# Kernel tuning notes

Measured on AMD Instinct MI355X. Metric: run time of the kernel, lower is better.

The kernel has to match this reference:

```python
import jax, jax.numpy as jnp
import numpy as np

L, B, H, R = 128, 4, 768, 97
LN_EPS = 1e-5


def setup_inputs() -> dict:
    key = jax.random.key(0)
    ks = jax.random.split(key, 8)
    s = 0.02
    return {
        "h_re1": jax.random.normal(ks[0], (L, B, H), jnp.float32),
        "h_re2": jax.random.normal(ks[1], (L, B, H), jnp.float32),
        "mask": jax.random.uniform(ks[2], (L, B), jnp.float32),
        "Wr": jax.random.normal(ks[3], (H, 2 * H), jnp.float32) * s,
        "br": jnp.zeros((H,), jnp.float32),
        "Wh": jax.random.normal(ks[4], (H, 3 * H), jnp.float32) * s,
        "bh": jnp.zeros((H,), jnp.float32),
        "gamma": jnp.ones((H,), jnp.float32),
        "beta": jnp.zeros((H,), jnp.float32),
        "Wo": jax.random.normal(ks[5], (R, H), jnp.float32) * s,
        "bo": jnp.zeros((R,), jnp.float32),
    }


def reference(h_re1, h_re2, mask, Wr, br, Wh, bh, gamma, beta, Wo, bo):
    # h_re1, h_re2: [L, B, H]; mask: [L, B]
    h = h_re2.shape[-1]
    # global context: tanh(Linear(cat(h_re1,h_re2))), max over length -> [B, H]
    g = jnp.tanh(jnp.einsum('lbi,hi->lbh', jnp.concatenate([h_re1, h_re2], axis=-1), Wr) + br)
    g = jnp.max(g, axis=0)  # [B, H]
    # hid2hid(cat(r1, r2, g)) == r1 @ W1.T + r2 @ W2.T + g @ W3.T + b
    # (avoids materializing the [L,L,B,3H] repeat+cat tensor)
    W1, W2, W3 = Wh[:, :h], Wh[:, h:2 * h], Wh[:, 2 * h:]
    a = jnp.einsum('lbi,hi->lbh', h_re2, W1)          # varies over first pair axis
    b2 = jnp.einsum('lbi,hi->lbh', h_re2, W2)         # varies over second pair axis
    gp = jnp.einsum('bi,hi->bh', g, W3) + bh          # constant over pairs
    pre = a[:, None, :, :] + b2[None, :, :, :] + gp   # [L, L, B, H]
    # LayerNorm over last dim (biased variance, as in torch)
    mu = jnp.mean(pre, axis=-1, keepdims=True)
    var = jnp.var(pre, axis=-1, keepdims=True)
    x = (pre - mu) * jax.lax.rsqrt(var + LN_EPS) * gamma + beta
    x = jax.nn.elu(x)  # dropout is identity in eval mode
    out = jax.nn.sigmoid(jnp.einsum('klbh,rh->klbr', x, Wo) + bo)  # [L, L, B, R]
    # pairwise mask: mask_e1 * mask_e2, broadcast over relation dim
    m = mask[:, None, :, None] * mask[None, :, :, None]
    return out * m
```

## Files before the change

### kernel.cpp

```cpp
#include <hip/hip_runtime.h>
#include <hip/hip_bf16.h>
#include <stdint.h>

#define L_ 128
#define B_ 4
#define H_ 768
#define R_ 97
#define LN_EPS 1e-5f

typedef _Float16 f16x8 __attribute__((ext_vector_type(8)));
typedef _Float16 f16x4 __attribute__((ext_vector_type(4)));
typedef _Float16 f16x2 __attribute__((ext_vector_type(2)));
typedef float f32x4 __attribute__((ext_vector_type(4)));

extern "C" __device__ _Float16 __ocml_exp2_f16(_Float16);

__device__ inline f16x8 cvt8(float4 v0, float4 v1) {
  f16x8 o;
  o[0] = (_Float16)v0.x; o[1] = (_Float16)v0.y; o[2] = (_Float16)v0.z; o[3] = (_Float16)v0.w;
  o[4] = (_Float16)v1.x; o[5] = (_Float16)v1.y; o[6] = (_Float16)v1.z; o[7] = (_Float16)v1.w;
  return o;
}

__global__ __launch_bounds__(256) void prep_all(const float* __restrict__ h1,
                                                const float* __restrict__ h2,
                                                const float* __restrict__ Wr,
                                                const float* __restrict__ Wh,
                                                const float* __restrict__ Wo,
                                                const float* __restrict__ gamma,
                                                const float* __restrict__ beta,
                                                _Float16* __restrict__ ccH,
                                                _Float16* __restrict__ BpR,
                                                _Float16* __restrict__ BpW,
                                                _Float16* __restrict__ WoP,
                                                _Float16* __restrict__ gbH,
                                                unsigned int* __restrict__ gmaxU) {
  int blk = blockIdx.x;
  if (blk < 512) {
    const float2* s1 = (const float2*)(h1 + (size_t)blk * H_);
    const float2* s2 = (const float2*)(h2 + (size_t)blk * H_);
    f16x2* d = (f16x2*)(ccH + (size_t)blk * (2 * H_));
    for (int i = threadIdx.x; i < H_ / 2; i += 256) {
      float2 v = s1[i]; f16x2 o; o[0] = (_Float16)v.x; o[1] = (_Float16)v.y; d[i] = o;
    }
    for (int i = threadIdx.x; i < H_ / 2; i += 256) {
      float2 v = s2[i]; f16x2 o; o[0] = (_Float16)v.x; o[1] = (_Float16)v.y; d[H_ / 2 + i] = o;
    }
    return;
  }
  blk -= 512;
  if (blk < 576) {
    int c = blk * 256 + threadIdx.x;
    int l = c & 63, u = c >> 6;
    int nt = u % 48, ks = u / 48;
    int n = nt * 16 + (l & 15);
    int k = ks * 32 + ((l >> 4) << 3);
    const float4* s = (const float4*)(Wr + (size_t)n * 1536 + k);
    *(f16x8*)(BpR + (size_t)c * 8) = cvt8(s[0], s[1]);
    return;
  }
  blk -= 576;
  if (blk < 576) {
    int c = blk * 256 + threadIdx.x;
    int l = c & 63, u = c >> 6;
    int nt = u % 96, ks = u / 96;
    int n = nt * 16 + (l & 15);
    int k = ks * 32 + ((l >> 4) << 3);
    const float* src = (n < 768) ? (Wh + (size_t)n * 2304 + k)
                                 : (Wh + (size_t)(n - 768) * 2304 + 768 + k);
    const float4* s = (const float4*)src;
    *(f16x8*)(BpW + (size_t)c * 8) = cvt8(s[0], s[1]);
    return;
  }
  blk -= 576;
  if (blk < 48) {
    int c = blk * 256 + threadIdx.x;
    int l = c & 63, u = c >> 6;
    int nt = u & 7, ks = u >> 3;
    int n = nt * 16 + (l & 15);
    int k = ks * 32 + ((l >> 4) << 3);
    f16x8 o = {};
    if (n < R_) {
      const float4* s = (const float4*)(Wo + (size_t)n * 768 + k);
      o = cvt8(s[0], s[1]);
    }
    *(f16x8*)(WoP + (size_t)c * 8) = o;
    return;
  }
  blk -= 48;
  if (blk < 3) {
    int i = blk * 256 + threadIdx.x;
    if (i < H_) {
      gbH[i] = (_Float16)gamma[i];
      gbH[H_ + i] = (_Float16)beta[i];
    }
    return;
  }
  blk -= 3;
  int i = blk * 256 + threadIdx.x;
  if (i < B_ * H_) gmaxU[i] = 0u;
}

__device__ __forceinline__ void gemm_g_tile(int nb, int mb,
                                            const _Float16* __restrict__ A,
                                            const _Float16* __restrict__ BpR,
                                            const float* __restrict__ br,
                                            unsigned int* __restrict__ gmaxU) {
  int w = threadIdx.x >> 6, l = threadIdx.x & 63;
  int row0 = mb * 32 + (w & 1) * 16;
  int nt0 = nb * 4 + (w >> 1) * 2;
  const f16x8* ap = (const f16x8*)(A + (size_t)(row0 + (l & 15)) * 1536 + (l >> 4) * 8);
  const f16x8* bp = (const f16x8*)(BpR + ((size_t)nt0 * 64 + l) * 8);
  f32x4 acc0 = {}, acc1 = {};
  f16x8 ac = ap[0], b0c = bp[0], b1c = bp[64];
  for (int ks = 0; ks < 48; ++ks) {
    f16x8 an = {}, b0n = {}, b1n = {};
    if (ks < 47) {
      an = ap[(ks + 1) * 4];
      b0n = bp[(size_t)(ks + 1) * 3072];
      b1n = bp[(size_t)(ks + 1) * 3072 + 64];
    }
    acc0 = __builtin_amdgcn_mfma_f32_16x16x32_f16(ac, b0c, acc0, 0, 0, 0);
    acc1 = __builtin_amdgcn_mfma_f32_16x16x32_f16(ac, b1c, acc1, 0, 0, 0);
    ac = an; b0c = b0n; b1c = b1n;
  }
#pragma unroll
  for (int q = 0; q < 2; ++q) {
    f32x4 acc = q ? acc1 : acc0;
    int col = nb * 64 + (w >> 1) * 32 + q * 16 + (l & 15);
#pragma unroll
    for (int r = 0; r < 4; ++r) {
      int row = row0 + (l >> 4) * 4 + r;
      float t = tanhf(acc[r] + br[col]) + 1.0f;
      atomicMax(&gmaxU[(row & 3) * H_ + col], __float_as_uint(t));
    }
  }
}

__device__ __forceinline__ void gemm_ab_tile(int nb, int mb,
                                             const _Float16* __restrict__ ccH,
                                             const _Float16* __restrict__ BpW,
                                             _Float16* __restrict__ aH,
                                             _Float16* __restrict__ bH) {
  int w = threadIdx.x >> 6, l = threadIdx.x & 63;
  int row0 = mb * 32 + (w & 1) * 16;
  int nt0 = nb * 4 + (w >> 1) * 2;
  const f16x8* ap = (const f16x8*)(ccH + (size_t)(row0 + (l & 15)) * 1536 + 768 + (l >> 4) * 8);
  const f16x8* bp = (const f16x8*)(BpW + ((size_t)nt0 * 64 + l) * 8);
  f32x4 acc0 = {}, acc1 = {};
  f16x8 ac = ap[0], b0c = bp[0], b1c = bp[64];
  for (int ks = 0; ks < 24; ++ks) {
    f16x8 an = {}, b0n = {}, b1n = {};
    if (ks < 23) {
      an = ap[(ks + 1) * 4];
      b0n = bp[(size_t)(ks + 1) * 6144];
      b1n = bp[(size_t)(ks + 1) * 6144 + 64];
    }
    acc0 = __builtin_amdgcn_mfma_f32_16x16x32_f16(ac, b0c, acc0, 0, 0, 0);
    acc1 = __builtin_amdgcn_mfma_f32_16x16x32_f16(ac, b1c, acc1, 0, 0, 0);
    ac = an; b0c = b0n; b1c = b1n;
  }
#pragma unroll
  for (int q = 0; q < 2; ++q) {
    f32x4 acc = q ? acc1 : acc0;
    int col = nb * 64 + (w >> 1) * 32 + q * 16 + (l & 15);
#pragma unroll
    for (int r = 0; r < 4; ++r) {
      int row = row0 + (l >> 4) * 4 + r;
      float v = acc[r];
      if (col < 768) aH[(size_t)row * H_ + col] = (_Float16)v;
      else           bH[(size_t)row * H_ + (col - 768)] = (_Float16)v;
    }
  }
}

__global__ __launch_bounds__(256) void gemm_both(const _Float16* __restrict__ ccH,
                                                 const _Float16* __restrict__ BpR,
                                                 const _Float16* __restrict__ BpW,
                                                 const float* __restrict__ br,
                                                 unsigned int* __restrict__ gmaxU,
                                                 _Float16* __restrict__ aH,
                                                 _Float16* __restrict__ bH) {
  int bid = blockIdx.x;
  if (bid < 192) {
    gemm_g_tile(bid % 12, bid / 12, ccH, BpR, br, gmaxU);
  } else {
    int j2 = bid - 192;
    gemm_ab_tile(j2 % 24, j2 / 24, ccH, BpW, aH, bH);
  }
}

__global__ __launch_bounds__(256) void gp_kernel(const float* __restrict__ Wh,
                                                 const unsigned int* __restrict__ gmaxU,
                                                 const float* __restrict__ bh,
                                                 float* __restrict__ gpv) {
  int n = blockIdx.x;
  int w = threadIdx.x >> 6, l = threadIdx.x & 63;
  const float* wr = Wh + (size_t)n * 2304 + 1536;
  const unsigned int* gm = gmaxU + (size_t)w * H_;
  float s = 0.f;
#pragma unroll
  for (int t = 0; t < 12; ++t) {
    int i = l + 64 * t;
    s += wr[i] * (__uint_as_float(gm[i]) - 1.0f);
  }
#pragma unroll
  for (int off = 32; off; off >>= 1) s += __shfl_xor(s, off);
  if (l == 0) gpv[(size_t)w * H_ + n] = s + bh[n];
}

__global__ __launch_bounds__(256) void stats(const _Float16* __restrict__ aH,
                                             const _Float16* __restrict__ bH,
                                             const float* __restrict__ gpv,
                                             _Float16* __restrict__ aH2,
                                             float* __restrict__ S,
                                             float* __restrict__ Q) {
  int r = blockIdx.x * 4 + (threadIdx.x >> 6);
  int l = threadIdx.x & 63;
  float s = 0.f, q = 0.f;
  if (r < 512) {
    int b = r & 3;
    const f16x4* ap = (const f16x4*)(aH + (size_t)r * H_);
    const float4* gp4 = (const float4*)(gpv + (size_t)b * H_);
    f16x4* op = (f16x4*)(aH2 + (size_t)r * H_);
#pragma unroll
    for (int t = 0; t < 3; ++t) {
      int i = t * 64 + l;
      f16x4 av = ap[i];
      float4 g4 = gp4[i];
      f16x4 o;
      o[0] = (_Float16)((float)av[0] + g4.x);
      o[1] = (_Float16)((float)av[1] + g4.y);
      o[2] = (_Float16)((float)av[2] + g4.z);
      o[3] = (_Float16)((float)av[3] + g4.w);
      op[i] = o;
#pragma unroll
      for (int j = 0; j < 4; ++j) { float y = (float)o[j]; s += y; q += y * y; }
    }
  } else {
    const f16x4* bp = (const f16x4*)(bH + (size_t)(r - 512) * H_);
#pragma unroll
    for (int t = 0; t < 3; ++t) {
      f16x4 bv = bp[t * 64 + l];
#pragma unroll
      for (int j = 0; j < 4; ++j) { float y = (float)bv[j]; s += y; q += y * y; }
    }
  }
#pragma unroll
  for (int off = 32; off; off >>= 1) {
    s += __shfl_xor(s, off);
    q += __shfl_xor(q, off);
  }
  if (l == 0) { S[r] = s; Q[r] = q; }
}

__global__ __launch_bounds__(256) void dotab(const _Float16* __restrict__ aH2,
                                             const _Float16* __restrict__ bH,
                                             const float* __restrict__ S,
                                             const float* __restrict__ Q,
                                             float* __restrict__ mu_arr,
                                             float* __restrict__ rs_arr) {
  int w = threadIdx.x >> 6, l = threadIdx.x & 63;
  int ltq = blockIdx.x, kt = blockIdx.y, b = blockIdx.z;
  int lt = ltq * 4 + w;
  const f16x8* ap = (const f16x8*)(aH2 + ((size_t)(kt * 16 + (l & 15)) * 4 + b) * H_ + (l >> 4) * 8);
  const f16x8* bp = (const f16x8*)(bH + ((size_t)(lt * 16 + (l & 15)) * 4 + b) * H_ + (l >> 4) * 8);
  f32x4 acc = {};
  f16x8 a0 = ap[0], b0 = bp[0], a1 = ap[4], b1 = bp[4];
  for (int ks = 0; ks < 24; ++ks) {
    f16x8 a2 = {}, b2 = {};
    if (ks < 22) { a2 = ap[(ks + 2) * 4]; b2 = bp[(ks + 2) * 4]; }
    acc = __builtin_amdgcn_mfma_f32_16x16x32_f16(a0, b0, acc, 0, 0, 0);
    a0 = a1; b0 = b1; a1 = a2; b1 = b2;
  }
#pragma unroll
  for (int r = 0; r < 4; ++r) {
    int k = kt * 16 + (l >> 4) * 4 + r;
    int lg = lt * 16 + (l & 15);
    int arow = k * 4 + b, brow = lg * 4 + b;
    float mu = (S[arow] + S[512 + brow]) * (1.f / H_);
    float q2 = Q[arow] + Q[512 + brow] + 2.f * acc[r];
    float var = fmaxf(q2 * (1.f / H_) - mu * mu, 0.f);
    float rs = rsqrtf(var + LN_EPS);
    size_t idx = (size_t)k * 512 + (size_t)lg * 4 + b;
    mu_arr[idx] = mu;
    rs_arr[idx] = rs;
  }
}

__global__ __launch_bounds__(256) void fused2(const _Float16* __restrict__ aH2,
                                              const _Float16* __restrict__ bH,
                                              const _Float16* __restrict__ gbH,
                                              const _Float16* __restrict__ WoP,
                                              const float* __restrict__ bo,
                                              const float* __restrict__ mask,
                                              const float* __restrict__ mu_arr,
                                              const float* __restrict__ rs_arr,
                                              float* __restrict__ out) {
  __shared__ __align__(16) uint4 WoLds[2048];
  int tid = threadIdx.x, w = tid >> 6, l = tid & 63;
  int m0 = blockIdx.x * 64;
  int myrow = m0 + w * 16 + (l & 15);
  int b = myrow & 3, li = (myrow >> 2) & 127, kk = myrow >> 9;
  const f16x8* ap = (const f16x8*)(aH2 + ((size_t)kk * 4 + b) * H_ + (l >> 4) * 8);
  const f16x8* bp = (const f16x8*)(bH + ((size_t)li * 4 + b) * H_ + (l >> 4) * 8);
  const f16x8* gp8 = (const f16x8*)(gbH + (l >> 4) * 8);
  const f16x8* be8 = (const f16x8*)(gbH + H_ + (l >> 4) * 8);
  float mu = mu_arr[myrow], rs = rs_arr[myrow];
  _Float16 muh = (_Float16)mu, rsh = (_Float16)rs;
  _Float16 l2e = (_Float16)1.44269504f;
  f16x8 mu8, rs8, zero8, one8, l2e8;
#pragma unroll
  for (int j = 0; j < 8; ++j) {
    mu8[j] = muh; rs8[j] = rsh;
    zero8[j] = (_Float16)0.f; one8[j] = (_Float16)1.f; l2e8[j] = l2e;
  }

  const uint4* wog = (const uint4*)WoP;
  f16x8 a8 = ap[0], b8 = bp[0], g8 = gp8[0], e8 = be8[0];

  f32x4 acc[7] = {};
  for (int ph = 0; ph < 6; ++ph) {
    __syncthreads();
    const uint4* gsrc = wog + (size_t)ph * 2048;
#pragma unroll
    for (int g = 0; g < 2; ++g) {
      uint4 v0 = gsrc[(g * 4 + 0) * 256 + tid];
      uint4 v1 = gsrc[(g * 4 + 1) * 256 + tid];
      uint4 v2 = gsrc[(g * 4 + 2) * 256 + tid];
      uint4 v3 = gsrc[(g * 4 + 3) * 256 + tid];
      WoLds[(g * 4 + 0) * 256 + tid] = v0;
      WoLds[(g * 4 + 1) * 256 + tid] = v1;
      WoLds[(g * 4 + 2) * 256 + tid] = v2;
      WoLds[(g * 4 + 3) * 256 + tid] = v3;
    }
    __syncthreads();
#pragma unroll
    for (int s = 0; s < 4; ++s) {
      int ks = ph * 4 + s;
      f16x8 an = {}, bn = {}, gn = {}, en = {};
      if (ks < 23) {
        an = ap[(ks + 1) * 4];
        bn = bp[(ks + 1) * 4];
        gn = gp8[(ks + 1) * 4];
        en = be8[(ks + 1) * 4];
      }
      f16x8 x = a8 + b8;
      f16x8 c1 = rs8 * g8;
      f16x8 yv = (x - mu8) * c1 + e8;
      f16x8 y2 = yv * l2e8;
      f16x8 ex;
#pragma unroll
      for (int j = 0; j < 8; ++j) ex[j] = __ocml_exp2_f16(y2[j]);
      ex = ex - one8;
      f16x8 av = __builtin_elementwise_max(yv, zero8) + __builtin_elementwise_min(ex, zero8);
      const f16x8* bvp = (const f16x8*)&WoLds[s * 512];
#pragma unroll
      for (int q = 0; q < 7; ++q) {
        f16x8 bv = bvp[q * 64 + l];
        acc[q] = __builtin_amdgcn_mfma_f32_16x16x32_f16(av, bv, acc[q], 0, 0, 0);
      }
      a8 = an; b8 = bn; g8 = gn; e8 = en;
    }
  }
  float mv[4];
#pragma unroll
  for (int r = 0; r < 4; ++r) {
    int row = m0 + w * 16 + (l >> 4) * 4 + r;
    int bb = row & 3, ll = (row >> 2) & 127, kx = row >> 9;
    mv[r] = mask[kx * 4 + bb] * mask[ll * 4 + bb];
  }
#pragma unroll
  for (int q = 0; q < 7; ++q) {
    int col = q * 16 + (l & 15);
    if (col < R_) {
      float bov = bo[col];
#pragma unroll
      for (int r = 0; r < 4; ++r) {
        int row = m0 + w * 16 + (l >> 4) * 4 + r;
        float z = acc[q][r] + bov;
        out[(size_t)row * R_ + col] = mv[r] / (1.f + __expf(-z));
      }
    }
  }
}

extern "C" void kernel_launch(void* const* d_in, const int* in_sizes, int n_in,
                              void* d_out, int out_size, void* d_ws, size_t ws_size,
                              hipStream_t stream) {
  const float* h1    = (const float*)d_in[0];
  const float* h2    = (const float*)d_in[1];
  const float* mask  = (const float*)d_in[2];
  const float* Wr    = (const float*)d_in[3];
  const float* br    = (const float*)d_in[4];
  const float* Wh    = (const float*)d_in[5];
  const float* bh    = (const float*)d_in[6];
  const float* gamma = (const float*)d_in[7];
  const float* beta  = (const float*)d_in[8];
  const float* Wo    = (const float*)d_in[9];
  const float* bo    = (const float*)d_in[10];
  float* out = (float*)d_out;
  char* ws = (char*)d_ws;

  _Float16* ccH = (_Float16*)ws;                    size_t off = 512 * 1536 * 2;
  _Float16* BpR = (_Float16*)(ws + off);            off += (size_t)1536 * 768 * 2;
  _Float16* BpW = (_Float16*)(ws + off);            off += (size_t)768 * 1536 * 2;
  _Float16* WoP = (_Float16*)(ws + off);            off += 768 * 128 * 2;
  _Float16* gbH = (_Float16*)(ws + off);            off += 4096;
  _Float16* aH  = (_Float16*)(ws + off);            off += 512 * 768 * 2;
  _Float16* bH  = (_Float16*)(ws + off);            off += 512 * 768 * 2;
  _Float16* aH2 = (_Float16*)(ws + off);            off += 512 * 768 * 2;
  unsigned int* gmaxU = (unsigned int*)(ws + off);  off += 3072 * 4;
  float* gpv = (float*)(ws + off);                  off += 3072 * 4;
  float* S   = (float*)(ws + off);                  off += 1024 * 4;
  float* Q   = (float*)(ws + off);                  off += 1024 * 4;
  float* mu_arr = (float*)(ws + off);               off += 65536 * 4;
  float* rs_arr = (float*)(ws + off);               off += 65536 * 4;

  prep_all<<<512 + 576 + 576 + 48 + 3 + 12, 256, 0, stream>>>(h1, h2, Wr, Wh, Wo, gamma, beta,
                                                              ccH, BpR, BpW, WoP, gbH, gmaxU);

  gemm_both<<<576, 256, 0, stream>>>(ccH, BpR, BpW, br, gmaxU, aH, bH);
  gp_kernel<<<768, 256, 0, stream>>>(Wh, gmaxU, bh, gpv);
  stats<<<256, 256, 0, stream>>>(aH, bH, gpv, aH2, S, Q);
  dotab<<<dim3(2, 8, 4), 256, 0, stream>>>(aH2, bH, S, Q, mu_arr, rs_arr);

  fused2<<<1024, 256, 0, stream>>>(aH2, bH, gbH, WoP, bo, mask, mu_arr, rs_arr, out);
}
```

Before: 92.12 us.

## Fuse LayerNorm statistics into the output kernel, dropping stats and dotab launches

Removes the separate stats and dotab kernels. Each fused3 block now computes the per-row sums, squared sums and a-b dot products for its 64 pair rows directly from aH, bH and an fp16 gp vector, then derives mean and rstd in-block. The gp vector is added inside the main loop rather than pre-materialised into aH2. This saves two launches and the mu/rs round trip through global memory. In exchange every block redundantly recomputes stats with a serial 48-iteration loop per thread, and gp is now rounded to fp16 before the add.

```diff
diff --git a/kernel.cpp b/kernel.cpp
--- a/kernel.cpp
+++ b/kernel.cpp
@@ -193,7 +193,7 @@
 __global__ __launch_bounds__(256) void gp_kernel(const float* __restrict__ Wh,
                                                  const unsigned int* __restrict__ gmaxU,
                                                  const float* __restrict__ bh,
-                                                 float* __restrict__ gpv) {
+                                                 _Float16* __restrict__ gpH) {
   int n = blockIdx.x;
   int w = threadIdx.x >> 6, l = threadIdx.x & 63;
   const float* wr = Wh + (size_t)n * 2304 + 1536;
@@ -206,107 +206,83 @@
   }
 #pragma unroll
   for (int off = 32; off; off >>= 1) s += __shfl_xor(s, off);
-  if (l == 0) gpv[(size_t)w * H_ + n] = s + bh[n];
-}
-
-__global__ __launch_bounds__(256) void stats(const _Float16* __restrict__ aH,
-                                             const _Float16* __restrict__ bH,
-                                             const float* __restrict__ gpv,
-                                             _Float16* __restrict__ aH2,
-                                             float* __restrict__ S,
-                                             float* __restrict__ Q) {
-  int r = blockIdx.x * 4 + (threadIdx.x >> 6);
-  int l = threadIdx.x & 63;
-  float s = 0.f, q = 0.f;
-  if (r < 512) {
-    int b = r & 3;
-    const f16x4* ap = (const f16x4*)(aH + (size_t)r * H_);
-    const float4* gp4 = (const float4*)(gpv + (size_t)b * H_);
-    f16x4* op = (f16x4*)(aH2 + (size_t)r * H_);
-#pragma unroll
-    for (int t = 0; t < 3; ++t) {
-      int i = t * 64 + l;
-      f16x4 av = ap[i];
-      float4 g4 = gp4[i];
-      f16x4 o;
-      o[0] = (_Float16)((float)av[0] + g4.x);
-      o[1] = (_Float16)((float)av[1] + g4.y);
-      o[2] = (_Float16)((float)av[2] + g4.z);
-      o[3] = (_Float16)((float)av[3] + g4.w);
-      op[i] = o;
-#pragma unroll
-      for (int j = 0; j < 4; ++j) { float y = (float)o[j]; s += y; q += y * y; }
-    }
-  } else {
-    const f16x4* bp = (const f16x4*)(bH + (size_t)(r - 512) * H_);
-#pragma unroll
-    for (int t = 0; t < 3; ++t) {
-      f16x4 bv = bp[t * 64 + l];
-#pragma unroll
-      for (int j = 0; j < 4; ++j) { float y = (float)bv[j]; s += y; q += y * y; }
-    }
-  }
-#pragma unroll
-  for (int off = 32; off; off >>= 1) {
-    s += __shfl_xor(s, off);
-    q += __shfl_xor(q, off);
-  }
-  if (l == 0) { S[r] = s; Q[r] = q; }
-}
-
-__global__ __launch_bounds__(256) void dotab(const _Float16* __restrict__ aH2,
-                                             const _Float16* __restrict__ bH,
-                                             const float* __restrict__ S,
-                                             const float* __restrict__ Q,
-                                             float* __restrict__ mu_arr,
-                                             float* __restrict__ rs_arr) {
-  int w = threadIdx.x >> 6, l = threadIdx.x & 63;
-  int ltq = blockIdx.x, kt = blockIdx.y, b = blockIdx.z;
-  int lt = ltq * 4 + w;
-  const f16x8* ap = (const f16x8*)(aH2 + ((size_t)(kt * 16 + (l & 15)) * 4 + b) * H_ + (l >> 4) * 8);
-  const f16x8* bp = (const f16x8*)(bH + ((size_t)(lt * 16 + (l & 15)) * 4 + b) * H_ + (l >> 4) * 8);
-  f32x4 acc = {};
-  f16x8 a0 = ap[0], b0 = bp[0], a1 = ap[4], b1 = bp[4];
-  for (int ks = 0; ks < 24; ++ks) {
-    f16x8 a2 = {}, b2 = {};
-    if (ks < 22) { a2 = ap[(ks + 2) * 4]; b2 = bp[(ks + 2) * 4]; }
-    acc = __builtin_amdgcn_mfma_f32_16x16x32_f16(a0, b0, acc, 0, 0, 0);
-    a0 = a1; b0 = b1; a1 = a2; b1 = b2;
-  }
-#pragma unroll
-  for (int r = 0; r < 4; ++r) {
-    int k = kt * 16 + (l >> 4) * 4 + r;
-    int lg = lt * 16 + (l & 15);
-    int arow = k * 4 + b, brow = lg * 4 + b;
-    float mu = (S[arow] + S[512 + brow]) * (1.f / H_);
-    float q2 = Q[arow] + Q[512 + brow] + 2.f * acc[r];
-    float var = fmaxf(q2 * (1.f / H_) - mu * mu, 0.f);
-    float rs = rsqrtf(var + LN_EPS);
-    size_t idx = (size_t)k * 512 + (size_t)lg * 4 + b;
-    mu_arr[idx] = mu;
-    rs_arr[idx] = rs;
-  }
-}
-
-__global__ __launch_bounds__(256) void fused2(const _Float16* __restrict__ aH2,
+  if (l == 0) gpH[(size_t)w * H_ + n] = (_Float16)(s + bh[n]);
+}
+
+__global__ __launch_bounds__(256) void fused3(const _Float16* __restrict__ aH,
                                               const _Float16* __restrict__ bH,
+                                              const _Float16* __restrict__ gpH,
                                               const _Float16* __restrict__ gbH,
                                               const _Float16* __restrict__ WoP,
                                               const float* __restrict__ bo,
                                               const float* __restrict__ mask,
-                                              const float* __restrict__ mu_arr,
-                                              const float* __restrict__ rs_arr,
                                               float* __restrict__ out) {
   __shared__ __align__(16) uint4 WoLds[2048];
+  __shared__ float SA[4], QA[4], pS[64], pQ[64], pD[64];
   int tid = threadIdx.x, w = tid >> 6, l = tid & 63;
   int m0 = blockIdx.x * 64;
-  int myrow = m0 + w * 16 + (l & 15);
-  int b = myrow & 3, li = (myrow >> 2) & 127, kk = myrow >> 9;
-  const f16x8* ap = (const f16x8*)(aH2 + ((size_t)kk * 4 + b) * H_ + (l >> 4) * 8);
+  int kk = m0 >> 9;
+  int li0 = (m0 >> 2) & 127;
+
+  {
+    const f16x4* ar = (const f16x4*)(aH + ((size_t)(kk * 4 + w)) * H_);
+    const f16x4* gr = (const f16x4*)(gpH + (size_t)w * H_);
+    float s = 0.f, q = 0.f;
+#pragma unroll
+    for (int t = 0; t < 3; ++t) {
+      int i = t * 64 + l;
+      f16x4 a4 = ar[i], g4 = gr[i];
+#pragma unroll
+      for (int j = 0; j < 4; ++j) {
+        float x = (float)a4[j] + (float)g4[j];
+        s += x; q += x * x;
+      }
+    }
+#pragma unroll
+    for (int off = 32; off; off >>= 1) { s += __shfl_xor(s, off); q += __shfl_xor(q, off); }
+    if (l == 0) { SA[w] = s; QA[w] = q; }
+  }
+  {
+    int p = tid >> 2, sub = tid & 3;
+    int lig = p & 15;
+    int pb = (p >> 4);
+    int li = li0 + (p >> 2);
+    int b = p & 3;
+    (void)lig; (void)pb;
+    const f16x4* brp = (const f16x4*)(bH + ((size_t)li * 4 + b) * H_);
+    const f16x4* arp = (const f16x4*)(aH + ((size_t)(kk * 4 + b)) * H_);
+    const f16x4* grp = (const f16x4*)(gpH + (size_t)b * H_);
+    float sb = 0.f, qb = 0.f, d = 0.f;
+    for (int i = 0; i < 48; ++i) {
+      int idx = sub + 4 * i;
+      f16x4 b4 = brp[idx], a4 = arp[idx], g4 = grp[idx];
+#pragma unroll
+      for (int j = 0; j < 4; ++j) {
+        float bv = (float)b4[j];
+        float av = (float)a4[j] + (float)g4[j];
+        sb += bv; qb += bv * bv; d += av * bv;
+      }
+    }
+    sb += __shfl_xor(sb, 1); sb += __shfl_xor(sb, 2);
+    qb += __shfl_xor(qb, 1); qb += __shfl_xor(qb, 2);
+    d  += __shfl_xor(d, 1);  d  += __shfl_xor(d, 2);
+    if (sub == 0) { pS[p] = sb; pQ[p] = qb; pD[p] = d; }
+  }
+  __syncthreads();
+  int rr = w * 16 + (l & 15);
+  int b = rr & 3;
+  int pair = rr;
+  float mu = (SA[b] + pS[pair]) * (1.f / H_);
+  float q2 = QA[b] + pQ[pair] + 2.f * pD[pair];
+  float var = fmaxf(q2 * (1.f / H_) - mu * mu, 0.f);
+  float rs = rsqrtf(var + LN_EPS);
+
+  int li = li0 + (rr >> 2);
+  const f16x8* ap = (const f16x8*)(aH + ((size_t)(kk * 4 + b)) * H_ + (l >> 4) * 8);
   const f16x8* bp = (const f16x8*)(bH + ((size_t)li * 4 + b) * H_ + (l >> 4) * 8);
+  const f16x8* gpp = (const f16x8*)(gpH + (size_t)b * H_ + (l >> 4) * 8);
   const f16x8* gp8 = (const f16x8*)(gbH + (l >> 4) * 8);
   const f16x8* be8 = (const f16x8*)(gbH + H_ + (l >> 4) * 8);
-  float mu = mu_arr[myrow], rs = rs_arr[myrow];
   _Float16 muh = (_Float16)mu, rsh = (_Float16)rs;
   _Float16 l2e = (_Float16)1.44269504f;
   f16x8 mu8, rs8, zero8, one8, l2e8;
@@ -317,7 +293,7 @@
   }
 
   const uint4* wog = (const uint4*)WoP;
-  f16x8 a8 = ap[0], b8 = bp[0], g8 = gp8[0], e8 = be8[0];
+  f16x8 a8 = ap[0], b8 = bp[0], p8 = gpp[0], g8 = gp8[0], e8 = be8[0];
 
   f32x4 acc[7] = {};
   for (int ph = 0; ph < 6; ++ph) {
@@ -338,14 +314,15 @@
 #pragma unroll
     for (int s = 0; s < 4; ++s) {
       int ks = ph * 4 + s;
-      f16x8 an = {}, bn = {}, gn = {}, en = {};
+      f16x8 an = {}, bn = {}, pn = {}, gn = {}, en = {};
       if (ks < 23) {
         an = ap[(ks + 1) * 4];
         bn = bp[(ks + 1) * 4];
+        pn = gpp[(ks + 1) * 4];
         gn = gp8[(ks + 1) * 4];
         en = be8[(ks + 1) * 4];
       }
-      f16x8 x = a8 + b8;
+      f16x8 x = (a8 + b8) + p8;
       f16x8 c1 = rs8 * g8;
       f16x8 yv = (x - mu8) * c1 + e8;
       f16x8 y2 = yv * l2e8;
@@ -360,7 +337,7 @@
         f16x8 bv = bvp[q * 64 + l];
         acc[q] = __builtin_amdgcn_mfma_f32_16x16x32_f16(av, bv, acc[q], 0, 0, 0);
       }
-      a8 = an; b8 = bn; g8 = gn; e8 = en;
+      a8 = an; b8 = bn; p8 = pn; g8 = gn; e8 = en;
     }
   }
   float mv[4];
@@ -409,21 +386,14 @@
   _Float16* gbH = (_Float16*)(ws + off);            off += 4096;
   _Float16* aH  = (_Float16*)(ws + off);            off += 512 * 768 * 2;
   _Float16* bH  = (_Float16*)(ws + off);            off += 512 * 768 * 2;
-  _Float16* aH2 = (_Float16*)(ws + off);            off += 512 * 768 * 2;
   unsigned int* gmaxU = (unsigned int*)(ws + off);  off += 3072 * 4;
-  float* gpv = (float*)(ws + off);                  off += 3072 * 4;
-  float* S   = (float*)(ws + off);                  off += 1024 * 4;
-  float* Q   = (float*)(ws + off);                  off += 1024 * 4;
-  float* mu_arr = (float*)(ws + off);               off += 65536 * 4;
-  float* rs_arr = (float*)(ws + off);               off += 65536 * 4;
+  _Float16* gpH = (_Float16*)(ws + off);            off += 4 * 768 * 2;
 
   prep_all<<<512 + 576 + 576 + 48 + 3 + 12, 256, 0, stream>>>(h1, h2, Wr, Wh, Wo, gamma, beta,
                                                               ccH, BpR, BpW, WoP, gbH, gmaxU);
 
   gemm_both<<<576, 256, 0, stream>>>(ccH, BpR, BpW, br, gmaxU, aH, bH);
-  gp_kernel<<<768, 256, 0, stream>>>(Wh, gmaxU, bh, gpv);
-  stats<<<256, 256, 0, stream>>>(aH, bH, gpv, aH2, S, Q);
-  dotab<<<dim3(2, 8, 4), 256, 0, stream>>>(aH2, bH, S, Q, mu_arr, rs_arr);
-
-  fused2<<<1024, 256, 0, stream>>>(aH2, bH, gbH, WoP, bo, mask, mu_arr, rs_arr, out);
-}
+  gp_kernel<<<768, 256, 0, stream>>>(Wh, gmaxU, bh, gpH);
+
+  fused3<<<1024, 256, 0, stream>>>(aH, bH, gpH, gbH, WoP, bo, mask, out);
+}
```

New measurement: 124.7 us. 35.4% more time.

## Process two 16-row tiles per wave in fused2 to reuse staged Wo

Applied to the files above, without the earlier changes.

Each block of fused2 now covers 128 rows instead of 64, with every wave computing two 16-row MFMA tiles that share each Wo fragment read from LDS. The grid halves to 512 blocks, so the global-to-LDS staging of Wo is done half as often per row. The software prefetch of the next k-slice of a/b/gamma/beta is dropped in favour of direct loads in the loop. The cost is doubled accumulator registers, which may lower occupancy and expose load latency.

```diff
diff --git a/kernel.cpp b/kernel.cpp
--- a/kernel.cpp
+++ b/kernel.cpp
@@ -299,27 +299,33 @@
                                               float* __restrict__ out) {
   __shared__ __align__(16) uint4 WoLds[2048];
   int tid = threadIdx.x, w = tid >> 6, l = tid & 63;
-  int m0 = blockIdx.x * 64;
-  int myrow = m0 + w * 16 + (l & 15);
-  int b = myrow & 3, li = (myrow >> 2) & 127, kk = myrow >> 9;
-  const f16x8* ap = (const f16x8*)(aH2 + ((size_t)kk * 4 + b) * H_ + (l >> 4) * 8);
-  const f16x8* bp = (const f16x8*)(bH + ((size_t)li * 4 + b) * H_ + (l >> 4) * 8);
+  int m0 = blockIdx.x * 128;
+  int kk = m0 >> 9;
+  int row0 = m0 + w * 32 + (l & 15);
+  int row1 = row0 + 16;
+  int b0 = row0 & 3, li0 = (row0 >> 2) & 127;
+  int b1 = row1 & 3, li1 = (row1 >> 2) & 127;
+  const f16x8* ap0 = (const f16x8*)(aH2 + ((size_t)kk * 4 + b0) * H_ + (l >> 4) * 8);
+  const f16x8* bp0 = (const f16x8*)(bH + ((size_t)li0 * 4 + b0) * H_ + (l >> 4) * 8);
+  const f16x8* ap1 = (const f16x8*)(aH2 + ((size_t)kk * 4 + b1) * H_ + (l >> 4) * 8);
+  const f16x8* bp1 = (const f16x8*)(bH + ((size_t)li1 * 4 + b1) * H_ + (l >> 4) * 8);
   const f16x8* gp8 = (const f16x8*)(gbH + (l >> 4) * 8);
   const f16x8* be8 = (const f16x8*)(gbH + H_ + (l >> 4) * 8);
-  float mu = mu_arr[myrow], rs = rs_arr[myrow];
-  _Float16 muh = (_Float16)mu, rsh = (_Float16)rs;
+  float mu0f = mu_arr[row0], rs0f = rs_arr[row0];
+  float mu1f = mu_arr[row1], rs1f = rs_arr[row1];
   _Float16 l2e = (_Float16)1.44269504f;
-  f16x8 mu8, rs8, zero8, one8, l2e8;
+  f16x8 mu80, rs80, mu81, rs81, zero8, one8, l2e8;
 #pragma unroll
   for (int j = 0; j < 8; ++j) {
-    mu8[j] = muh; rs8[j] = rsh;
+    mu80[j] = (_Float16)mu0f; rs80[j] = (_Float16)rs0f;
+    mu81[j] = (_Float16)mu1f; rs81[j] = (_Float16)rs1f;
     zero8[j] = (_Float16)0.f; one8[j] = (_Float16)1.f; l2e8[j] = l2e;
   }
 
   const uint4* wog = (const uint4*)WoP;
-  f16x8 a8 = ap[0], b8 = bp[0], g8 = gp8[0], e8 = be8[0];
-
-  f32x4 acc[7] = {};
+
+  f32x4 acc0[7] = {};
+  f32x4 acc1[7] = {};
   for (int ph = 0; ph < 6; ++ph) {
     __syncthreads();
     const uint4* gsrc = wog + (size_t)ph * 2048;
@@ -338,48 +344,60 @@
 #pragma unroll
     for (int s = 0; s < 4; ++s) {
       int ks = ph * 4 + s;
-      f16x8 an = {}, bn = {}, gn = {}, en = {};
-      if (ks < 23) {
-        an = ap[(ks + 1) * 4];
-        bn = bp[(ks + 1) * 4];
-        gn = gp8[(ks + 1) * 4];
-        en = be8[(ks + 1) * 4];
+      f16x8 a80 = ap0[ks * 4];
+      f16x8 b80 = bp0[ks * 4];
+      f16x8 a81 = ap1[ks * 4];
+      f16x8 b81 = bp1[ks * 4];
+      f16x8 g8 = gp8[ks * 4];
+      f16x8 e8 = be8[ks * 4];
+      f16x8 x0 = a80 + b80;
+      f16x8 x1 = a81 + b81;
+      f16x8 c10 = rs80 * g8;
+      f16x8 c11 = rs81 * g8;
+      f16x8 yv0 = (x0 - mu80) * c10 + e8;
+      f16x8 yv1 = (x1 - mu81) * c11 + e8;
+      f16x8 y20 = yv0 * l2e8;
+      f16x8 y21 = yv1 * l2e8;
+      f16x8 ex0, ex1;
+#pragma unroll
+      for (int j = 0; j < 8; ++j) {
+        ex0[j] = __ocml_exp2_f16(y20[j]);
+        ex1[j] = __ocml_exp2_f16(y21[j]);
       }
-      f16x8 x = a8 + b8;
-      f16x8 c1 = rs8 * g8;
-      f16x8 yv = (x - mu8) * c1 + e8;
-      f16x8 y2 = yv * l2e8;
-      f16x8 ex;
-#pragma unroll
-      for (int j = 0; j < 8; ++j) ex[j] = __ocml_exp2_f16(y2[j]);
-      ex = ex - one8;
-      f16x8 av = __builtin_elementwise_max(yv, zero8) + __builtin_elementwise_min(ex, zero8);
+      ex0 = ex0 - one8;
+      ex1 = ex1 - one8;
+      f16x8 av0 = __builtin_elementwise_max(yv0, zero8) + __builtin_elementwise_min(ex0, zero8);
+      f16x8 av1 = __builtin_elementwise_max(yv1, zero8) + __builtin_elementwise_min(ex1, zero8);
       const f16x8* bvp = (const f16x8*)&WoLds[s * 512];
 #pragma unroll
       for (int q = 0; q < 7; ++q) {
         f16x8 bv = bvp[q * 64 + l];
-        acc[q] = __builtin_amdgcn_mfma_f32_16x16x32_f16(av, bv, acc[q], 0, 0, 0);
+        acc0[q] = __builtin_amdgcn_mfma_f32_16x16x32_f16(av0, bv, acc0[q], 0, 0, 0);
+        acc1[q] = __builtin_amdgcn_mfma_f32_16x16x32_f16(av1, bv, acc1[q], 0, 0, 0);
       }
-      a8 = an; b8 = bn; g8 = gn; e8 = en;
-    }
-  }
-  float mv[4];
-#pragma unroll
-  for (int r = 0; r < 4; ++r) {
-    int row = m0 + w * 16 + (l >> 4) * 4 + r;
-    int bb = row & 3, ll = (row >> 2) & 127, kx = row >> 9;
-    mv[r] = mask[kx * 4 + bb] * mask[ll * 4 + bb];
-  }
-#pragma unroll
-  for (int q = 0; q < 7; ++q) {
-    int col = q * 16 + (l & 15);
-    if (col < R_) {
-      float bov = bo[col];
-#pragma unroll
-      for (int r = 0; r < 4; ++r) {
-        int row = m0 + w * 16 + (l >> 4) * 4 + r;
-        float z = acc[q][r] + bov;
-        out[(size_t)row * R_ + col] = mv[r] / (1.f + __expf(-z));
+    }
+  }
+#pragma unroll
+  for (int set = 0; set < 2; ++set) {
+    int rbase = m0 + w * 32 + set * 16;
+    float mv[4];
+#pragma unroll
+    for (int r = 0; r < 4; ++r) {
+      int row = rbase + (l >> 4) * 4 + r;
+      int bb = row & 3, ll = (row >> 2) & 127, kx = row >> 9;
+      mv[r] = mask[kx * 4 + bb] * mask[ll * 4 + bb];
+    }
+#pragma unroll
+    for (int q = 0; q < 7; ++q) {
+      int col = q * 16 + (l & 15);
+      if (col < R_) {
+        float bov = bo[col];
+#pragma unroll
+        for (int r = 0; r < 4; ++r) {
+          int row = rbase + (l >> 4) * 4 + r;
+          float z = (set ? acc1[q][r] : acc0[q][r]) + bov;
+          out[(size_t)row * R_ + col] = mv[r] / (1.f + __expf(-z));
+        }
       }
     }
   }
@@ -425,5 +443,5 @@
   stats<<<256, 256, 0, stream>>>(aH, bH, gpv, aH2, S, Q);
   dotab<<<dim3(2, 8, 4), 256, 0, stream>>>(aH2, bH, S, Q, mu_arr, rs_arr);
 
-  fused2<<<1024, 256, 0, stream>>>(aH2, bH, gbH, WoP, bo, mask, mu_arr, rs_arr, out);
-}
+  fused2<<<512, 256, 0, stream>>>(aH2, bH, gbH, WoP, bo, mask, mu_arr, rs_arr, out);
+}
```

After: 87.12 us. 1.06x faster.
